# Kernel tuning notes

Hardware: AMD Instinct MI355X
Metric: run time of the kernel (lower is better)

Reference implementation:

```python
import jax, jax.numpy as jnp
import numpy as np

B, L, D, H = 2, 2048, 1024, 16
HD = D // H  # head dim = 64


def setup_inputs() -> dict:
    key = jax.random.key(0)
    ks = jax.random.split(key, 6)
    s = 0.02
    return {
        "hidden_states": jax.random.normal(ks[0], (B, L, D), jnp.float32),
        "attention_mask": jnp.zeros((B, 1, 1, L), jnp.float32),
        "Wq": jax.random.normal(ks[1], (D, D), jnp.float32) * s,
        "bq": jnp.zeros((D,), jnp.float32),
        "Wk": jax.random.normal(ks[2], (D, D), jnp.float32) * s,
        "bk": jnp.zeros((D,), jnp.float32),
        "Wv": jax.random.normal(ks[3], (D, D), jnp.float32) * s,
        "bv": jnp.zeros((D,), jnp.float32),
        "Wo": jax.random.normal(ks[4], (D, D), jnp.float32) * s,
        "bo": jnp.zeros((D,), jnp.float32),
    }


def reference(hidden_states, attention_mask, Wq, bq, Wk, bk, Wv, bv, Wo, bo):
    # Linear projections (torch Linear: x @ W.T + b; here W stored as [in,out])
    q = hidden_states @ Wq + bq  # [B,L,D]
    k = hidden_states @ Wk + bk
    v = hidden_states @ Wv + bv

    def split_heads(x):  # [B,L,D] -> [B,H,L,HD]
        return x.reshape(B, L, H, HD).transpose(0, 2, 1, 3)

    q, k, v = split_heads(q), split_heads(k), split_heads(v)

    scores = jnp.einsum("bhqd,bhkd->bhqk", q, k) / jnp.sqrt(
        jnp.asarray(HD, q.dtype)
    )
    scores = scores + attention_mask  # additive mask, broadcast [B,1,1,L]
    pdtype = scores.dtype
    # fp32 upcast around softmax, as in the original module
    probs = jax.nn.softmax(scores.astype(jnp.float32), axis=-1).astype(pdtype)
    # dropout prob = 0 (eval) -> identity; head_mask=None
    ctx = jnp.einsum("bhqk,bhkd->bhqd", probs, v)  # [B,H,L,HD]
    ctx = ctx.transpose(0, 2, 1, 3).reshape(B, L, D)
    out = ctx @ Wo + bo  # BertSelfOutput_preLN dense (dropout=0)
    return out
```

## Files before the change

### kernel.cpp

```cpp
#include <hip/hip_runtime.h>

#define BB 2
#define LL 2048
#define DDIM 1024
#define HH 16
#define HDIM 64
#define MM (BB*LL)
#define KK 1024
#define LOG2E 1.44269504f

typedef __attribute__((ext_vector_type(8))) short s8v;
typedef __attribute__((ext_vector_type(4))) float f4v;

__device__ __forceinline__ unsigned short f2bf(float f) {
    unsigned int u = __float_as_uint(f);
    u += 0x7fffu + ((u >> 16) & 1u);
    return (unsigned short)(u >> 16);
}

__device__ __forceinline__ float fexp2(float x) { return __builtin_amdgcn_exp2f(x); }

__device__ __forceinline__ void gld_lds16(const unsigned short* g, unsigned short* l) {
    __builtin_amdgcn_global_load_lds(
        (const __attribute__((address_space(1))) unsigned int*)g,
        (__attribute__((address_space(3))) unsigned int*)l, 16, 0, 0);
}

__global__ __launch_bounds__(256) void convert_x(const float* __restrict__ x,
                                                 unsigned short* __restrict__ xb) {
    int i = blockIdx.x * 256 + threadIdx.x;
    float4 v = ((const float4*)x)[i];
    ushort4 r;
    r.x = f2bf(v.x); r.y = f2bf(v.y); r.z = f2bf(v.z); r.w = f2bf(v.w);
    ((ushort4*)xb)[i] = r;
}

__global__ void transpose_w(const float* __restrict__ w0, const float* __restrict__ w1,
                            const float* __restrict__ w2, const float* __restrict__ w3,
                            unsigned short* __restrict__ o0, unsigned short* __restrict__ o1,
                            unsigned short* __restrict__ o2, unsigned short* __restrict__ o3) {
    const float* src; unsigned short* dst;
    switch (blockIdx.z) {
        case 0: src = w0; dst = o0; break;
        case 1: src = w1; dst = o1; break;
        case 2: src = w2; dst = o2; break;
        default: src = w3; dst = o3; break;
    }
    __shared__ float tile[32][33];
    int n0 = blockIdx.x * 32, k0 = blockIdx.y * 32;
    int tx = threadIdx.x, ty = threadIdx.y;
    #pragma unroll
    for (int j = 0; j < 4; ++j)
        tile[ty + j*8][tx] = src[(size_t)(k0 + ty + j*8) * DDIM + n0 + tx];
    __syncthreads();
    #pragma unroll
    for (int j = 0; j < 4; ++j)
        dst[(size_t)(n0 + ty + j*8) * KK + k0 + tx] = f2bf(tile[tx][ty + j*8]);
}

__device__ __forceinline__ void gemm_core(const unsigned short* __restrict__ A,
                                          const unsigned short* __restrict__ BT,
                                          int Mbase, int Nbase,
                                          unsigned short* As, unsigned short* Bs,
                                          f4v acc[4][4]) {
    const int t = threadIdx.x;
    const int lane = t & 63, wave = t >> 6;
    const int wm = wave & 1, wn = wave >> 1;
    const int l15 = lane & 15, quad = lane >> 4;
    const int srow = t >> 2, schunk = (t & 3) * 8;

    #pragma unroll
    for (int mt = 0; mt < 4; ++mt)
        #pragma unroll
        for (int nt = 0; nt < 4; ++nt)
            acc[mt][nt] = f4v{0.f, 0.f, 0.f, 0.f};

    const unsigned short* gA0 = A  + (size_t)(Mbase + srow)      * KK + schunk;
    const unsigned short* gA1 = A  + (size_t)(Mbase + 64 + srow) * KK + schunk;
    const unsigned short* gB0 = BT + (size_t)(Nbase + srow)      * KK + schunk;
    const unsigned short* gB1 = BT + (size_t)(Nbase + 64 + srow) * KK + schunk;
    unsigned short* lA0 = As + t*8;
    unsigned short* lA1 = As + 64*32 + t*8;
    unsigned short* lB0 = Bs + t*8;
    unsigned short* lB1 = Bs + 64*32 + t*8;

    for (int kb = 0; kb < KK; kb += 32) {
        __syncthreads();
        gld_lds16(gA0 + kb, lA0);
        gld_lds16(gA1 + kb, lA1);
        gld_lds16(gB0 + kb, lB0);
        gld_lds16(gB1 + kb, lB1);
        __syncthreads();
        s8v af[4], bfv[4];
        #pragma unroll
        for (int mt = 0; mt < 4; ++mt)
            af[mt] = *(const s8v*)(As + (wm*64 + mt*16 + l15)*32 + quad*8);
        #pragma unroll
        for (int nt = 0; nt < 4; ++nt)
            bfv[nt] = *(const s8v*)(Bs + (wn*64 + nt*16 + l15)*32 + quad*8);
        #pragma unroll
        for (int mt = 0; mt < 4; ++mt)
            #pragma unroll
            for (int nt = 0; nt < 4; ++nt)
                acc[mt][nt] = __builtin_amdgcn_mfma_f32_16x16x32_bf16(af[mt], bfv[nt], acc[mt][nt], 0, 0, 0);
    }
}

__global__ __launch_bounds__(256) void qkv_gemm(
        const unsigned short* __restrict__ Xb,
        const unsigned short* __restrict__ WqT, const unsigned short* __restrict__ WkT,
        const unsigned short* __restrict__ WvT,
        const float* __restrict__ bq, const float* __restrict__ bk, const float* __restrict__ bv,
        unsigned short* __restrict__ Qh, unsigned short* __restrict__ Kh,
        unsigned short* __restrict__ Vt) {
    __shared__ alignas(16) unsigned short As[128*32];
    __shared__ alignas(16) unsigned short Bs[128*32];
    const int mode = blockIdx.z;
    const unsigned short* BT = (mode == 0) ? WqT : (mode == 1) ? WkT : WvT;
    const float* bias        = (mode == 0) ? bq  : (mode == 1) ? bk  : bv;
    unsigned short* out      = (mode == 0) ? Qh  : (mode == 1) ? Kh  : Vt;
    const int Mbase = blockIdx.y * 128, Nbase = blockIdx.x * 128;

    f4v acc[4][4];
    gemm_core(Xb, BT, Mbase, Nbase, As, Bs, acc);

    const int lane = threadIdx.x & 63, wave = threadIdx.x >> 6;
    const int wm = wave & 1, wn = wave >> 1, l15 = lane & 15, quad = lane >> 4;
    #pragma unroll
    for (int mt = 0; mt < 4; ++mt)
        #pragma unroll
        for (int nt = 0; nt < 4; ++nt)
            #pragma unroll
            for (int r = 0; r < 4; ++r) {
                int gm = Mbase + wm*64 + mt*16 + quad*4 + r;
                int gn = Nbase + wn*64 + nt*16 + l15;
                float v = acc[mt][nt][r] + bias[gn];
                int bb = gm >> 11, ll = gm & 2047;
                int hh = gn >> 6,  dd = gn & 63;
                if (mode == 2)
                    out[((size_t)(bb*HH + hh)*HDIM + dd)*LL + ll] = f2bf(v);
                else
                    out[((size_t)(bb*HH + hh)*LL + ll)*HDIM + dd] = f2bf(v);
            }
}

__global__ __launch_bounds__(256) void attn(
        const unsigned short* __restrict__ Qh, const unsigned short* __restrict__ Kh,
        const unsigned short* __restrict__ Vt, const float* __restrict__ mask,
        unsigned short* __restrict__ ctx) {
    __shared__ alignas(16) unsigned short Ks[64*72];
    __shared__ alignas(16) unsigned short Vs[64*72];
    __shared__ alignas(16) unsigned short P [4*16*72];

    const int t = threadIdx.x, lane = t & 63, wave = t >> 6;
    const int l15 = lane & 15, quad = lane >> 4;

    const int n = blockIdx.x;
    const int bh = (n & 7) * 4 + ((n >> 3) & 3);
    const int qblk = n >> 5;
    const int b = bh >> 4, h = bh & 15;

    const unsigned short* Qb = Qh + (size_t)bh * LL * HDIM;
    const unsigned short* Kb = Kh + (size_t)bh * LL * HDIM;
    const unsigned short* Vb = Vt + (size_t)bh * HDIM * LL;
    const float* mb = mask + (size_t)b * LL;
    const int q0 = qblk * 64 + wave * 16;
    unsigned short* Pw = P + wave * 16 * 72;

    const int srow = t >> 2, scol = (t & 3) * 16;

    s8v qf[2];
    #pragma unroll
    for (int hf = 0; hf < 2; ++hf)
        qf[hf] = *(const s8v*)(Qb + (size_t)(q0 + l15)*HDIM + hf*32 + quad*8);

    f4v o[4];
    #pragma unroll
    for (int dt = 0; dt < 4; ++dt) o[dt] = f4v{0.f, 0.f, 0.f, 0.f};
    float rs[4];
    #pragma unroll
    for (int r = 0; r < 4; ++r) rs[r] = 0.f;

    const float C1 = 0.125f * LOG2E;

    for (int kt = 0; kt < LL; kt += 64) {
        float4 ka = *(const float4*)(Kb + (size_t)(kt + srow)*HDIM + scol);
        float4 kb2 = *(const float4*)(Kb + (size_t)(kt + srow)*HDIM + scol + 8);
        float4 va = *(const float4*)(Vb + (size_t)srow*LL + kt + scol);
        float4 vb2 = *(const float4*)(Vb + (size_t)srow*LL + kt + scol + 8);
        float mv[4];
        #pragma unroll
        for (int nt = 0; nt < 4; ++nt)
            mv[nt] = mb[kt + nt*16 + l15] * LOG2E;

        __syncthreads();
        *(float4*)(Ks + srow*72 + scol)     = ka;
        *(float4*)(Ks + srow*72 + scol + 8) = kb2;
        *(float4*)(Vs + srow*72 + scol)     = va;
        *(float4*)(Vs + srow*72 + scol + 8) = vb2;
        __syncthreads();

        f4v sac[4];
        #pragma unroll
        for (int nt = 0; nt < 4; ++nt) {
            sac[nt] = f4v{0.f, 0.f, 0.f, 0.f};
            #pragma unroll
            for (int hf = 0; hf < 2; ++hf) {
                s8v kf = *(const s8v*)(Ks + (nt*16 + l15)*72 + hf*32 + quad*8);
                sac[nt] = __builtin_amdgcn_mfma_f32_16x16x32_bf16(qf[hf], kf, sac[nt], 0, 0, 0);
            }
        }
        #pragma unroll
        for (int nt = 0; nt < 4; ++nt)
            #pragma unroll
            for (int r = 0; r < 4; ++r) {
                float p = fexp2(sac[nt][r] * C1 + mv[nt]);
                rs[r] += p;
                Pw[(quad*4 + r)*72 + nt*16 + l15] = f2bf(p);
            }
        s8v pf[2];
        #pragma unroll
        for (int hf = 0; hf < 2; ++hf)
            pf[hf] = *(const s8v*)(Pw + l15*72 + hf*32 + quad*8);
        #pragma unroll
        for (int dt = 0; dt < 4; ++dt)
            #pragma unroll
            for (int hf = 0; hf < 2; ++hf) {
                s8v vfr = *(const s8v*)(Vs + (dt*16 + l15)*72 + hf*32 + quad*8);
                o[dt] = __builtin_amdgcn_mfma_f32_16x16x32_bf16(pf[hf], vfr, o[dt], 0, 0, 0);
            }
    }

    #pragma unroll
    for (int r = 0; r < 4; ++r) {
        float s0 = rs[r];
        s0 += __shfl_xor(s0, 1);
        s0 += __shfl_xor(s0, 2);
        s0 += __shfl_xor(s0, 4);
        s0 += __shfl_xor(s0, 8);
        float inv = 1.0f / s0;
        int q = q0 + quad*4 + r;
        size_t base = ((size_t)b*LL + q)*DDIM + h*HDIM;
        #pragma unroll
        for (int dt = 0; dt < 4; ++dt)
            ctx[base + dt*16 + l15] = f2bf(o[dt][r] * inv);
    }
}

__global__ __launch_bounds__(256) void out_gemm(
        const unsigned short* __restrict__ Cb, const unsigned short* __restrict__ WoT,
        const float* __restrict__ bo, float* __restrict__ out) {
    __shared__ alignas(16) unsigned short As[128*32];
    __shared__ alignas(16) unsigned short Bs[128*32];
    const int Mbase = blockIdx.y * 128, Nbase = blockIdx.x * 128;
    f4v acc[4][4];
    gemm_core(Cb, WoT, Mbase, Nbase, As, Bs, acc);
    const int lane = threadIdx.x & 63, wave = threadIdx.x >> 6;
    const int wm = wave & 1, wn = wave >> 1, l15 = lane & 15, quad = lane >> 4;
    #pragma unroll
    for (int mt = 0; mt < 4; ++mt)
        #pragma unroll
        for (int nt = 0; nt < 4; ++nt)
            #pragma unroll
            for (int r = 0; r < 4; ++r) {
                int gm = Mbase + wm*64 + mt*16 + quad*4 + r;
                int gn = Nbase + wn*64 + nt*16 + l15;
                out[(size_t)gm*DDIM + gn] = acc[mt][nt][r] + bo[gn];
            }
}

extern "C" void kernel_launch(void* const* d_in, const int* in_sizes, int n_in,
                              void* d_out, int out_size, void* d_ws, size_t ws_size,
                              hipStream_t stream) {
    const float* X    = (const float*)d_in[0];
    const float* mask = (const float*)d_in[1];
    const float* Wq   = (const float*)d_in[2];
    const float* bq   = (const float*)d_in[3];
    const float* Wk   = (const float*)d_in[4];
    const float* bk   = (const float*)d_in[5];
    const float* Wv   = (const float*)d_in[6];
    const float* bv   = (const float*)d_in[7];
    const float* Wo   = (const float*)d_in[8];
    const float* bo   = (const float*)d_in[9];
    float* out = (float*)d_out;

    char* ws = (char*)d_ws;
    unsigned short* Xb  = (unsigned short*)(ws);
    unsigned short* WqT = (unsigned short*)(ws + (8u  << 20));
    unsigned short* WkT = (unsigned short*)(ws + (10u << 20));
    unsigned short* WvT = (unsigned short*)(ws + (12u << 20));
    unsigned short* WoT = (unsigned short*)(ws + (14u << 20));
    unsigned short* Qh  = (unsigned short*)(ws + (16u << 20));
    unsigned short* Kh  = (unsigned short*)(ws + (24u << 20));
    unsigned short* Vt  = (unsigned short*)(ws + (32u << 20));
    unsigned short* Cb  = Xb;

    convert_x  <<<dim3(4096),      dim3(256),   0, stream>>>(X, Xb);
    transpose_w<<<dim3(32,32,4),   dim3(32,8),  0, stream>>>(Wq, Wk, Wv, Wo, WqT, WkT, WvT, WoT);
    qkv_gemm   <<<dim3(8,32,3),    dim3(256),   0, stream>>>(Xb, WqT, WkT, WvT, bq, bk, bv, Qh, Kh, Vt);
    attn       <<<dim3(1024),      dim3(256),   0, stream>>>(Qh, Kh, Vt, mask, Cb);
    out_gemm   <<<dim3(8,32),      dim3(256),   0, stream>>>(Cb, WoT, bo, out);
}
```

Baseline: 225.8 us.

## Merge prep kernels, vectorize weight transpose, and halve out_gemm N tile

Folds the input conversion and weight transposes into one launch, which removes a kernel launch gap. The transpose now uses 64x64 tiles with float4 loads and 16-byte bf16 stores. The output GEMM switches to a 128x64 tile, so the grid grows from 256 to 512 blocks and fills the CUs better. The trade-off is less data reuse per block in the output GEMM and more LDS per transpose block.

```diff
diff --git a/kernel.cpp b/kernel.cpp
--- a/kernel.cpp
+++ b/kernel.cpp
@@ -10,6 +10,7 @@
 #define LOG2E 1.44269504f
 
 typedef __attribute__((ext_vector_type(8))) short s8v;
+typedef __attribute__((ext_vector_type(8))) unsigned short u8v;
 typedef __attribute__((ext_vector_type(4))) float f4v;
 
 __device__ __forceinline__ unsigned short f2bf(float f) {
@@ -26,36 +27,49 @@
         (__attribute__((address_space(3))) unsigned int*)l, 16, 0, 0);
 }
 
-__global__ __launch_bounds__(256) void convert_x(const float* __restrict__ x,
-                                                 unsigned short* __restrict__ xb) {
-    int i = blockIdx.x * 256 + threadIdx.x;
-    float4 v = ((const float4*)x)[i];
-    ushort4 r;
-    r.x = f2bf(v.x); r.y = f2bf(v.y); r.z = f2bf(v.z); r.w = f2bf(v.w);
-    ((ushort4*)xb)[i] = r;
-}
-
-__global__ void transpose_w(const float* __restrict__ w0, const float* __restrict__ w1,
-                            const float* __restrict__ w2, const float* __restrict__ w3,
-                            unsigned short* __restrict__ o0, unsigned short* __restrict__ o1,
-                            unsigned short* __restrict__ o2, unsigned short* __restrict__ o3) {
+__global__ __launch_bounds__(256) void prep(
+        const float* __restrict__ X,
+        const float* __restrict__ Wq, const float* __restrict__ Wk,
+        const float* __restrict__ Wv, const float* __restrict__ Wo,
+        unsigned short* __restrict__ Xb,
+        unsigned short* __restrict__ WqT, unsigned short* __restrict__ WkT,
+        unsigned short* __restrict__ WvT, unsigned short* __restrict__ WoT) {
+    __shared__ float lds[64][65];
+    const int blk = blockIdx.x, t = threadIdx.x;
+    if (blk < 4096) {
+        int i = blk * 256 + t;
+        float4 v = ((const float4*)X)[i];
+        ushort4 r;
+        r.x = f2bf(v.x); r.y = f2bf(v.y); r.z = f2bf(v.z); r.w = f2bf(v.w);
+        ((ushort4*)Xb)[i] = r;
+        return;
+    }
+    const int tb = blk - 4096;
+    const int w = tb >> 8;
+    const int tile = tb & 255;
+    const int k0 = (tile >> 4) * 64, n0 = (tile & 15) * 64;
     const float* src; unsigned short* dst;
-    switch (blockIdx.z) {
-        case 0: src = w0; dst = o0; break;
-        case 1: src = w1; dst = o1; break;
-        case 2: src = w2; dst = o2; break;
-        default: src = w3; dst = o3; break;
-    }
-    __shared__ float tile[32][33];
-    int n0 = blockIdx.x * 32, k0 = blockIdx.y * 32;
-    int tx = threadIdx.x, ty = threadIdx.y;
-    #pragma unroll
-    for (int j = 0; j < 4; ++j)
-        tile[ty + j*8][tx] = src[(size_t)(k0 + ty + j*8) * DDIM + n0 + tx];
+    switch (w) {
+        case 0: src = Wq; dst = WqT; break;
+        case 1: src = Wk; dst = WkT; break;
+        case 2: src = Wv; dst = WvT; break;
+        default: src = Wo; dst = WoT; break;
+    }
+    #pragma unroll
+    for (int j = 0; j < 4; ++j) {
+        int r = (t >> 4) + 16*j, c = (t & 15) * 4;
+        float4 v = *(const float4*)(src + (size_t)(k0 + r) * DDIM + n0 + c);
+        lds[r][c] = v.x; lds[r][c+1] = v.y; lds[r][c+2] = v.z; lds[r][c+3] = v.w;
+    }
     __syncthreads();
     #pragma unroll
-    for (int j = 0; j < 4; ++j)
-        dst[(size_t)(n0 + ty + j*8) * KK + k0 + tx] = f2bf(tile[tx][ty + j*8]);
+    for (int j = 0; j < 2; ++j) {
+        int rr = (t >> 3) + 32*j, cc = (t & 7) * 8;
+        u8v o;
+        #pragma unroll
+        for (int i = 0; i < 8; ++i) o[i] = f2bf(lds[cc + i][rr]);
+        *(u8v*)(dst + (size_t)(n0 + rr) * KK + k0 + cc) = o;
+    }
 }
 
 __device__ __forceinline__ void gemm_core(const unsigned short* __restrict__ A,
@@ -251,20 +265,56 @@
         const unsigned short* __restrict__ Cb, const unsigned short* __restrict__ WoT,
         const float* __restrict__ bo, float* __restrict__ out) {
     __shared__ alignas(16) unsigned short As[128*32];
-    __shared__ alignas(16) unsigned short Bs[128*32];
-    const int Mbase = blockIdx.y * 128, Nbase = blockIdx.x * 128;
-    f4v acc[4][4];
-    gemm_core(Cb, WoT, Mbase, Nbase, As, Bs, acc);
-    const int lane = threadIdx.x & 63, wave = threadIdx.x >> 6;
-    const int wm = wave & 1, wn = wave >> 1, l15 = lane & 15, quad = lane >> 4;
+    __shared__ alignas(16) unsigned short Bs[64*32];
+    const int t = threadIdx.x;
+    const int lane = t & 63, wave = t >> 6;
+    const int wm = wave & 1, wn = wave >> 1;
+    const int l15 = lane & 15, quad = lane >> 4;
+    const int srow = t >> 2, schunk = (t & 3) * 8;
+    const int Mbase = blockIdx.y * 128, Nbase = blockIdx.x * 64;
+
+    f4v acc[4][2];
     #pragma unroll
     for (int mt = 0; mt < 4; ++mt)
         #pragma unroll
-        for (int nt = 0; nt < 4; ++nt)
+        for (int nt = 0; nt < 2; ++nt)
+            acc[mt][nt] = f4v{0.f, 0.f, 0.f, 0.f};
+
+    const unsigned short* gA0 = Cb  + (size_t)(Mbase + srow)      * KK + schunk;
+    const unsigned short* gA1 = Cb  + (size_t)(Mbase + 64 + srow) * KK + schunk;
+    const unsigned short* gB0 = WoT + (size_t)(Nbase + srow)      * KK + schunk;
+    unsigned short* lA0 = As + t*8;
+    unsigned short* lA1 = As + 64*32 + t*8;
+    unsigned short* lB0 = Bs + t*8;
+
+    for (int kb = 0; kb < KK; kb += 32) {
+        __syncthreads();
+        gld_lds16(gA0 + kb, lA0);
+        gld_lds16(gA1 + kb, lA1);
+        gld_lds16(gB0 + kb, lB0);
+        __syncthreads();
+        s8v af[4], bfv[2];
+        #pragma unroll
+        for (int mt = 0; mt < 4; ++mt)
+            af[mt] = *(const s8v*)(As + (wm*64 + mt*16 + l15)*32 + quad*8);
+        #pragma unroll
+        for (int nt = 0; nt < 2; ++nt)
+            bfv[nt] = *(const s8v*)(Bs + (wn*32 + nt*16 + l15)*32 + quad*8);
+        #pragma unroll
+        for (int mt = 0; mt < 4; ++mt)
+            #pragma unroll
+            for (int nt = 0; nt < 2; ++nt)
+                acc[mt][nt] = __builtin_amdgcn_mfma_f32_16x16x32_bf16(af[mt], bfv[nt], acc[mt][nt], 0, 0, 0);
+    }
+
+    #pragma unroll
+    for (int mt = 0; mt < 4; ++mt)
+        #pragma unroll
+        for (int nt = 0; nt < 2; ++nt)
             #pragma unroll
             for (int r = 0; r < 4; ++r) {
                 int gm = Mbase + wm*64 + mt*16 + quad*4 + r;
-                int gn = Nbase + wn*64 + nt*16 + l15;
+                int gn = Nbase + wn*32 + nt*16 + l15;
                 out[(size_t)gm*DDIM + gn] = acc[mt][nt][r] + bo[gn];
             }
 }
@@ -295,9 +345,8 @@
     unsigned short* Vt  = (unsigned short*)(ws + (32u << 20));
     unsigned short* Cb  = Xb;
 
-    convert_x  <<<dim3(4096),      dim3(256),   0, stream>>>(X, Xb);
-    transpose_w<<<dim3(32,32,4),   dim3(32,8),  0, stream>>>(Wq, Wk, Wv, Wo, WqT, WkT, WvT, WoT);
-    qkv_gemm   <<<dim3(8,32,3),    dim3(256),   0, stream>>>(Xb, WqT, WkT, WvT, bq, bk, bv, Qh, Kh, Vt);
-    attn       <<<dim3(1024),      dim3(256),   0, stream>>>(Qh, Kh, Vt, mask, Cb);
-    out_gemm   <<<dim3(8,32),      dim3(256),   0, stream>>>(Cb, WoT, bo, out);
-}
+    prep     <<<dim3(5120),    dim3(256), 0, stream>>>(X, Wq, Wk, Wv, Wo, Xb, WqT, WkT, WvT, WoT);
+    qkv_gemm <<<dim3(8,32,3),  dim3(256), 0, stream>>>(Xb, WqT, WkT, WvT, bq, bk, bv, Qh, Kh, Vt);
+    attn     <<<dim3(1024),    dim3(256), 0, stream>>>(Qh, Kh, Vt, mask, Cb);
+    out_gemm <<<dim3(16,32),   dim3(256), 0, stream>>>(Cb, WoT, bo, out);
+}
```

Measured after the change: 220.3 us. 2.4% less time.
